# Optimization experiments

Measured on AMD Instinct MI355X. Metric: run time of the kernel, lower is better.

The kernel has to match this reference:

```python
import jax, jax.numpy as jnp
import numpy as np

T, D, F_, E, K = 8192, 1024, 4096, 8, 2


def setup_inputs() -> dict:
    key = jax.random.key(0)
    ks = jax.random.split(key, 5)
    s_d = 1.0 / np.sqrt(D)
    s_f = 1.0 / np.sqrt(F_)
    return {
        "x": jax.random.normal(ks[0], (T, D), dtype=jnp.float32),
        "gate_w": jax.random.normal(ks[1], (D, E), dtype=jnp.float32) * s_d,
        "w1": jax.random.normal(ks[2], (E, D, F_), dtype=jnp.float32) * s_d,  # up (gate proj)
        "w3": jax.random.normal(ks[3], (E, D, F_), dtype=jnp.float32) * s_d,  # up (value proj)
        "w2": jax.random.normal(ks[4], (E, F_, D), dtype=jnp.float32) * s_f,  # down proj
    }


def reference(x, gate_w, w1, w2, w3):
    # gate + top-k routing
    logits = x @ gate_w                                   # [T, E]
    top_w, top_idx = jax.lax.top_k(logits, K)             # [T, K]
    w = jax.nn.softmax(top_w.astype(jnp.float32), axis=-1).astype(x.dtype)
    # combine[t, e] = routing weight of token t for expert e (0 if unrouted)
    combine = jnp.sum(w[:, :, None] * jax.nn.one_hot(top_idx, E, dtype=x.dtype), axis=1)  # [T, E]
    # dense dispatch: each expert processes all tokens, masked by combine weight
    # (identical math to the torch gather/scatter loop: unrouted tokens get weight 0)
    out = jnp.zeros_like(x)
    for e in range(E):
        h = jax.nn.silu(x @ w1[e]) * (x @ w3[e])          # [T, F] SwiGLU
        out = out + combine[:, e:e + 1] * (h @ w2[e])     # [T, D]
    return out
```

## Files before the change

kernel.cpp:

```cpp
#include <hip/hip_runtime.h>
#include <stdint.h>

#define T_TOK 8192
#define D_DIM 1024
#define F_DIM 4096
#define E_NUM 8
#define RCAP  17408
#define MT    136

typedef __bf16 bf16;
typedef __bf16 bf16x8 __attribute__((ext_vector_type(8)));
typedef float  f32x4  __attribute__((ext_vector_type(4)));

typedef const __attribute__((address_space(1))) void* gptr1;
typedef __attribute__((address_space(3))) void* lptr3;

__device__ __forceinline__ void gload_lds16(const void* g, void* l) {
    __builtin_amdgcn_global_load_lds((gptr1)g, (lptr3)l, 16, 0, 0);
}

__device__ __forceinline__ unsigned short f2b(float f) {
    uint32_t u = __float_as_uint(f);
    u = (u + 0x7FFFu + ((u >> 16) & 1u)) >> 16;
    return (unsigned short)u;
}

__global__ __launch_bounds__(256) void trans_kernel(const float* __restrict__ src,
                                                    bf16* __restrict__ dst,
                                                    int R, int C, int mode) {
    __shared__ float lt[64 * 68];
    const int e  = blockIdx.z;
    const int c0 = blockIdx.x * 64;
    const int r0 = blockIdx.y * 64;
    const float* s = src + (size_t)e * R * C;
    unsigned short* dp = (unsigned short*)dst + (size_t)e * R * C * (mode ? 2 : 1);
    const int t  = threadIdx.x;
    const int tr = t >> 4;
    const int tc = (t & 15) * 4;
    #pragma unroll
    for (int rr = 0; rr < 4; ++rr) {
        const int r = tr + rr * 16;
        const float4 v = *(const float4*)(s + (size_t)(r0 + r) * C + c0 + tc);
        *(float4*)&lt[r * 68 + tc] = v;
    }
    __syncthreads();
    const int oc  = t >> 2;
    const int seg = (t & 3) * 16;
    __attribute__((aligned(16))) unsigned short ob[16];
    #pragma unroll
    for (int i = 0; i < 16; ++i) ob[i] = f2b(lt[(seg + i) * 68 + oc]);
    const int f  = c0 + oc;
    const int fr = mode ? ((f >> 5) * 64 + ((mode == 2) ? 32 : 0) + (f & 31)) : f;
    unsigned short* orow = dp + (size_t)fr * R + (r0 + seg);
    *(uint4*)(orow)     = *(const uint4*)&ob[0];
    *(uint4*)(orow + 8) = *(const uint4*)&ob[8];
}

__global__ __launch_bounds__(256) void gate_kernel(const float* __restrict__ x,
                                                   const float* __restrict__ gw,
                                                   int* __restrict__ tki,
                                                   float* __restrict__ tkw,
                                                   int* __restrict__ counts) {
    const int t    = blockIdx.x * 4 + (threadIdx.x >> 6);
    const int lane = threadIdx.x & 63;
    const float* xr = x + (size_t)t * D_DIM;
    float acc[E_NUM];
    #pragma unroll
    for (int e = 0; e < E_NUM; ++e) acc[e] = 0.f;
    for (int j = 0; j < 16; ++j) {
        const int d = lane + 64 * j;
        const float xv = xr[d];
        const float* g = gw + (size_t)d * E_NUM;
        #pragma unroll
        for (int e = 0; e < E_NUM; ++e) acc[e] += xv * g[e];
    }
    #pragma unroll
    for (int off = 32; off >= 1; off >>= 1) {
        #pragma unroll
        for (int e = 0; e < E_NUM; ++e) acc[e] += __shfl_xor(acc[e], off);
    }
    if (lane == 0) {
        int b0 = 0; float v0 = acc[0];
        #pragma unroll
        for (int e = 1; e < E_NUM; ++e) if (acc[e] > v0) { v0 = acc[e]; b0 = e; }
        int b1 = -1; float v1 = -1e30f;
        #pragma unroll
        for (int e = 0; e < E_NUM; ++e) if (e != b0 && acc[e] > v1) { v1 = acc[e]; b1 = e; }
        const float ex = expf(v1 - v0);
        const float w0 = 1.f / (1.f + ex);
        const float w1 = ex * w0;
        tki[t * 2]     = b0;  tkw[t * 2]     = w0;
        tki[t * 2 + 1] = b1;  tkw[t * 2 + 1] = w1;
        atomicAdd(&counts[b0], 1);
        atomicAdd(&counts[b1], 1);
    }
}

__global__ void scan_kernel(const int* __restrict__ counts, int* __restrict__ aoff,
                            int* __restrict__ cursor) {
    if (threadIdx.x == 0) {
        int off = 0;
        #pragma unroll
        for (int e = 0; e < E_NUM; ++e) {
            aoff[e]   = off;
            cursor[e] = off;
            off += (counts[e] + 127) & ~127;
        }
        aoff[E_NUM] = off;
    }
}

__global__ __launch_bounds__(256) void gather_kernel(const float* __restrict__ x,
                                                     const int* __restrict__ tki,
                                                     int* __restrict__ cursor,
                                                     int* __restrict__ s2r,
                                                     bf16* __restrict__ xp) {
    const int slot = blockIdx.x * 4 + (threadIdx.x >> 6);
    const int lane = threadIdx.x & 63;
    const int t = slot >> 1;
    int row = 0;
    if (lane == 0) {
        const int e = tki[slot];
        row = atomicAdd(&cursor[e], 1);
        s2r[slot] = row;
    }
    row = __shfl(row, 0);
    const float* xr = x + (size_t)t * D_DIM + lane * 16;
    unsigned short* dst = (unsigned short*)xp + (size_t)row * D_DIM + lane * 16;
    uint32_t u[8];
    #pragma unroll
    for (int q = 0; q < 4; ++q) {
        const float4 v = *(const float4*)(xr + q * 4);
        u[q * 2]     = (uint32_t)f2b(v.x) | ((uint32_t)f2b(v.y) << 16);
        u[q * 2 + 1] = (uint32_t)f2b(v.z) | ((uint32_t)f2b(v.w) << 16);
    }
    ((uint4*)dst)[0] = make_uint4(u[0], u[1], u[2], u[3]);
    ((uint4*)dst)[1] = make_uint4(u[4], u[5], u[6], u[7]);
}

__global__ __launch_bounds__(512, 2) void gemm1_kernel(const bf16* __restrict__ xp,
                                                       const bf16* __restrict__ wb13t,
                                                       bf16* __restrict__ hb,
                                                       const int* __restrict__ aoff,
                                                       const int* __restrict__ counts) {
    __shared__ __align__(16) char As[65536];
    __shared__ __align__(16) char Bs[65536];

    const int flat    = blockIdx.y * 32 + blockIdx.x;
    const int logical = (flat & 7) * 288 + (flat >> 3);
    const int nt      = logical & 31;
    int bm            = logical >> 5;

    int e = 0;
    for (; e < E_NUM; ++e) {
        const int nbi = (counts[e] + 255) >> 8;
        if (bm < nbi) break;
        bm -= nbi;
    }
    if (e >= E_NUM) return;
    const int m_base = aoff[e] + bm * 256;
    const int row_hi = aoff[e + 1];

    const int tid  = threadIdx.x;
    const int w    = tid >> 6;
    const int lane = tid & 63;
    const int wm   = w >> 2;
    const int wn   = w & 3;

    const int    lsub = lane >> 3;
    const size_t swz  = (size_t)(((lane & 7) ^ lsub) << 3);
    const bf16* Ag = xp    + (size_t)m_base * D_DIM;
    const bf16* Bg = wb13t + ((size_t)e * (2 * F_DIM) + (size_t)nt * 256) * D_DIM;
    char* sAd = As + w * 2048 + lane * 16;
    char* sBd = Bs + w * 2048 + lane * 16;
    const int rst = w * 16 + lsub;

#define G1_STAGE_A(cc, kt, h)                                                         \
    do {                                                                              \
        const size_t kcol = (size_t)(kt) * 64 + swz;                                  \
        gload_lds16(Ag + (size_t)((h) * 128 + rst) * D_DIM + kcol,                    \
                    sAd + (cc) * 32768 + (h) * 16384);                                \
        gload_lds16(Ag + (size_t)((h) * 128 + rst + 8) * D_DIM + kcol,                \
                    sAd + (cc) * 32768 + (h) * 16384 + 1024);                         \
    } while (0)
#define G1_STAGE_B(cc, kt, h)                                                         \
    do {                                                                              \
        const size_t kcol = (size_t)(kt) * 64 + swz;                                  \
        gload_lds16(Bg + (size_t)((h) * 128 + rst) * D_DIM + kcol,                    \
                    sBd + (cc) * 32768 + (h) * 16384);                                \
        gload_lds16(Bg + (size_t)((h) * 128 + rst + 8) * D_DIM + kcol,                \
                    sBd + (cc) * 32768 + (h) * 16384 + 1024);                         \
    } while (0)

    const int fm  = lane & 15;
    const int kq  = lane >> 4;
    const int kg0 = ((kq       ^ (fm & 7)) << 4);
    const int kg1 = (((4 | kq) ^ (fm & 7)) << 4);
    const char* Arb = As + wm * 16384 + fm * 128;
    const char* Brb = Bs + (wn >> 1) * 16384 + ((wn & 1) * 64 + fm) * 128;

    f32x4 acc[8][4] = {};
    bf16x8 aF[4][2], b0F[2][2], b1F[2][2];

    G1_STAGE_A(0, 0, 0); G1_STAGE_A(0, 0, 1);
    G1_STAGE_B(0, 0, 0); G1_STAGE_B(0, 0, 1);
    G1_STAGE_B(1, 1, 0); G1_STAGE_B(1, 1, 1);
    asm volatile("s_waitcnt vmcnt(4)" ::: "memory");
    __builtin_amdgcn_s_barrier();
    __builtin_amdgcn_sched_barrier(0);

    for (int u = 0; u < D_DIM / 64; ++u) {
        const int c = u & 1;
        const char* Ar = Arb + c * 32768;
        const char* Br = Brb + c * 32768;

        #pragma unroll
        for (int i = 0; i < 4; ++i) {
            aF[i][0] = *(const bf16x8*)(Ar + i * 2048 + kg0);
            aF[i][1] = *(const bf16x8*)(Ar + i * 2048 + kg1);
        }
        #pragma unroll
        for (int j = 0; j < 2; ++j) {
            b0F[j][0] = *(const bf16x8*)(Br + j * 2048 + kg0);
            b0F[j][1] = *(const bf16x8*)(Br + j * 2048 + kg1);
        }
        if (u + 1 < D_DIM / 64) G1_STAGE_A(c ^ 1, u + 1, 0);
        __builtin_amdgcn_s_barrier();
        asm volatile("s_waitcnt lgkmcnt(0)" ::: "memory");
        __builtin_amdgcn_s_setprio(1);
        #pragma unroll
        for (int i = 0; i < 4; ++i)
            #pragma unroll
            for (int j = 0; j < 2; ++j) {
                acc[i][j] = __builtin_amdgcn_mfma_f32_16x16x32_bf16(aF[i][0], b0F[j][0], acc[i][j], 0, 0, 0);
                acc[i][j] = __builtin_amdgcn_mfma_f32_16x16x32_bf16(aF[i][1], b0F[j][1], acc[i][j], 0, 0, 0);
            }
        __builtin_amdgcn_s_setprio(0);
        __builtin_amdgcn_s_barrier();

        #pragma unroll
        for (int j = 0; j < 2; ++j) {
            b1F[j][0] = *(const bf16x8*)(Br + (j + 2) * 2048 + kg0);
            b1F[j][1] = *(const bf16x8*)(Br + (j + 2) * 2048 + kg1);
        }
        if (u + 1 < D_DIM / 64) G1_STAGE_A(c ^ 1, u + 1, 1);
        __builtin_amdgcn_s_barrier();
        asm volatile("s_waitcnt lgkmcnt(0)" ::: "memory");
        __builtin_amdgcn_s_setprio(1);
        #pragma unroll
        for (int i = 0; i < 4; ++i)
            #pragma unroll
            for (int j = 0; j < 2; ++j) {
                acc[i][j + 2] = __builtin_amdgcn_mfma_f32_16x16x32_bf16(aF[i][0], b1F[j][0], acc[i][j + 2], 0, 0, 0);
                acc[i][j + 2] = __builtin_amdgcn_mfma_f32_16x16x32_bf16(aF[i][1], b1F[j][1], acc[i][j + 2], 0, 0, 0);
            }
        __builtin_amdgcn_s_setprio(0);
        __builtin_amdgcn_s_barrier();

        #pragma unroll
        for (int i = 0; i < 4; ++i) {
            aF[i][0] = *(const bf16x8*)(Ar + (i + 4) * 2048 + kg0);
            aF[i][1] = *(const bf16x8*)(Ar + (i + 4) * 2048 + kg1);
        }
        if (u + 2 < D_DIM / 64) G1_STAGE_B(c, u + 2, 0);
        __builtin_amdgcn_s_barrier();
        asm volatile("s_waitcnt lgkmcnt(0)" ::: "memory");
        __builtin_amdgcn_s_setprio(1);
        #pragma unroll
        for (int i = 0; i < 4; ++i)
            #pragma unroll
            for (int j = 0; j < 2; ++j) {
                acc[i + 4][j] = __builtin_amdgcn_mfma_f32_16x16x32_bf16(aF[i][0], b0F[j][0], acc[i + 4][j], 0, 0, 0);
                acc[i + 4][j] = __builtin_amdgcn_mfma_f32_16x16x32_bf16(aF[i][1], b0F[j][1], acc[i + 4][j], 0, 0, 0);
            }
        __builtin_amdgcn_s_setprio(0);
        __builtin_amdgcn_s_barrier();

        if (u + 2 < D_DIM / 64) G1_STAGE_B(c, u + 2, 1);
        __builtin_amdgcn_s_setprio(1);
        #pragma unroll
        for (int i = 0; i < 4; ++i)
            #pragma unroll
            for (int j = 0; j < 2; ++j) {
                acc[i + 4][j + 2] = __builtin_amdgcn_mfma_f32_16x16x32_bf16(aF[i][0], b1F[j][0], acc[i + 4][j + 2], 0, 0, 0);
                acc[i + 4][j + 2] = __builtin_amdgcn_mfma_f32_16x16x32_bf16(aF[i][1], b1F[j][1], acc[i + 4][j + 2], 0, 0, 0);
            }
        __builtin_amdgcn_s_setprio(0);

        if (u == D_DIM / 64 - 1) break;
        if (u + 2 < D_DIM / 64) {
            asm volatile("s_waitcnt vmcnt(4)" ::: "memory");
        } else {
            asm volatile("s_waitcnt vmcnt(0)" ::: "memory");
        }
        __builtin_amdgcn_s_barrier();
        __builtin_amdgcn_sched_barrier(0);
    }

    unsigned short* hw = (unsigned short*)hb;
    const int g    = nt * 4 + wn;
    const int colb = g * 32 + fm;
    const int rb0  = m_base + wm * 128 + (kq << 2);
    #pragma unroll
    for (int i = 0; i < 8; ++i) {
        #pragma unroll
        for (int r = 0; r < 4; ++r) {
            const int row = rb0 + i * 16 + r;
            if (row < row_hi) {
                #pragma unroll
                for (int jj = 0; jj < 2; ++jj) {
                    const float s1 = acc[i][jj][r];
                    const float s3 = acc[i][jj + 2][r];
                    const float hv = (s1 / (1.0f + __expf(-s1))) * s3;
                    hw[(size_t)row * F_DIM + colb + jj * 16] = f2b(hv);
                }
            }
        }
    }
#undef G1_STAGE_A
#undef G1_STAGE_B
}

__global__ __launch_bounds__(256, 2) void gemm2_kernel(const bf16* __restrict__ hb,
                                                       const bf16* __restrict__ wb2t,
                                                       float* __restrict__ yb,
                                                       const int* __restrict__ aoff,
                                                       const int* __restrict__ counts) {
    __shared__ bf16 As[128 * 32];
    __shared__ bf16 Bs[128 * 32];

    const int flat    = blockIdx.y * 8 + blockIdx.x;
    const int logical = (flat & 7) * 136 + (flat >> 3);
    const int nt      = logical & 7;
    const int m_base  = (logical >> 3) * 128;

    int e = 0;
    #pragma unroll
    for (int i = 1; i < E_NUM; ++i) if (m_base >= aoff[i]) e = i;
    if (m_base - aoff[e] >= counts[e]) return;

    const int tid  = threadIdx.x;
    const int w    = tid >> 6;
    const int lane = tid & 63;
    const int wm   = w & 1, wn = w >> 1;

    const bf16* Ab = hb + (size_t)m_base * F_DIM;
    const bf16* Bb = wb2t + ((size_t)e * D_DIM + (size_t)nt * 128) * F_DIM;

    const int lr16 = lane >> 2;
    const int cg   = lane & 3;
    const int srow = w * 32 + lr16;
    const int scol = (cg ^ ((lr16 >> 1) & 3)) * 8;
    const int ldsbase = w * 1024;
    const int fm = lane & 15;
    const int fk = (((lane >> 4) ^ ((fm >> 1) & 3))) * 8;

    f32x4 acc[4][4] = {};

    for (int kt = 0; kt < F_DIM / 32; ++kt) {
        const int k0 = kt * 32;
        #pragma unroll
        for (int j = 0; j < 2; ++j) {
            const size_t go = (size_t)(srow + j * 16) * F_DIM + (k0 + scol);
            gload_lds16(Ab + go, &As[ldsbase + j * 512]);
            gload_lds16(Bb + go, &Bs[ldsbase + j * 512]);
        }
        __syncthreads();
        bf16x8 af[4], bfr[4];
        #pragma unroll
        for (int i = 0; i < 4; ++i) {
            af[i]  = *(const bf16x8*)&As[(wm * 64 + i * 16 + fm) * 32 + fk];
            bfr[i] = *(const bf16x8*)&Bs[(wn * 64 + i * 16 + fm) * 32 + fk];
        }
        #pragma unroll
        for (int i = 0; i < 4; ++i) {
            #pragma unroll
            for (int jn = 0; jn < 4; ++jn) {
                acc[i][jn] = __builtin_amdgcn_mfma_f32_16x16x32_bf16(af[i], bfr[jn], acc[i][jn], 0, 0, 0);
            }
        }
        __syncthreads();
    }

    #pragma unroll
    for (int i = 0; i < 4; ++i) {
        const int rb = m_base + wm * 64 + i * 16 + (lane >> 4) * 4;
        #pragma unroll
        for (int r = 0; r < 4; ++r) {
            float* yrow = yb + (size_t)(rb + r) * D_DIM;
            #pragma unroll
            for (int jn = 0; jn < 4; ++jn) {
                const int col = nt * 128 + wn * 64 + jn * 16 + (lane & 15);
                yrow[col] = acc[i][jn][r];
            }
        }
    }
}

__global__ __launch_bounds__(256) void combine_kernel(const float* __restrict__ yb,
                                                      const int* __restrict__ s2r,
                                                      const float* __restrict__ tkw,
                                                      float* __restrict__ out) {
    const int idx = blockIdx.x * 256 + threadIdx.x;
    const int t = idx >> 8;
    const int c = (idx & 255) * 4;
    const int r0 = s2r[t * 2], r1 = s2r[t * 2 + 1];
    const float w0 = tkw[t * 2], w1 = tkw[t * 2 + 1];
    const float4 a = *(const float4*)(yb + (size_t)r0 * D_DIM + c);
    const float4 b = *(const float4*)(yb + (size_t)r1 * D_DIM + c);
    float4 o;
    o.x = w0 * a.x + w1 * b.x;
    o.y = w0 * a.y + w1 * b.y;
    o.z = w0 * a.z + w1 * b.z;
    o.w = w0 * a.w + w1 * b.w;
    *(float4*)(out + (size_t)t * D_DIM + c) = o;
}

extern "C" void kernel_launch(void* const* d_in, const int* in_sizes, int n_in,
                              void* d_out, int out_size, void* d_ws, size_t ws_size,
                              hipStream_t stream) {
    const float* x  = (const float*)d_in[0];
    const float* gw = (const float*)d_in[1];
    const float* w1 = (const float*)d_in[2];
    const float* w3 = (const float*)d_in[3];
    const float* w2 = (const float*)d_in[4];
    float* out = (float*)d_out;

    char* ws = (char*)d_ws;
    bf16*  wb13t = (bf16*)(ws);
    bf16*  wb2t  = (bf16*)(ws);
    float* yb    = (float*)(ws + (size_t)67108864);
    bf16*  xp    = (bf16*)(ws + (size_t)134217728);
    size_t off   = (size_t)134217728 + (size_t)RCAP * D_DIM * 2;
    bf16*  hb    = (bf16*)(ws + off); off += (size_t)RCAP * F_DIM * 2;
    int*   tki = (int*)(ws + off);   off += (size_t)T_TOK * 2 * 4;
    float* tkw = (float*)(ws + off); off += (size_t)T_TOK * 2 * 4;
    int* counts = (int*)(ws + off);  off += 64;
    int* cursor = (int*)(ws + off);  off += 64;
    int* aoff   = (int*)(ws + off);  off += 64;
    int* s2r    = (int*)(ws + off);  off += (size_t)T_TOK * 2 * 4;

    hipMemsetAsync(counts, 0, 64, stream);

    gate_kernel<<<T_TOK / 4, 256, 0, stream>>>(x, gw, tki, tkw, counts);
    scan_kernel<<<1, 64, 0, stream>>>(counts, aoff, cursor);
    gather_kernel<<<(T_TOK * 2) / 4, 256, 0, stream>>>(x, tki, cursor, s2r, xp);

    trans_kernel<<<dim3(F_DIM / 64, D_DIM / 64, E_NUM), 256, 0, stream>>>(w1, wb13t, D_DIM, F_DIM, 1);
    trans_kernel<<<dim3(F_DIM / 64, D_DIM / 64, E_NUM), 256, 0, stream>>>(w3, wb13t, D_DIM, F_DIM, 2);

    gemm1_kernel<<<dim3(2 * F_DIM / 256, 72), 512, 0, stream>>>(xp, wb13t, hb, aoff, counts);

    trans_kernel<<<dim3(D_DIM / 64, F_DIM / 64, E_NUM), 256, 0, stream>>>(w2, wb2t, F_DIM, D_DIM, 0);

    gemm2_kernel<<<dim3(D_DIM / 128, MT), 256, 0, stream>>>(hb, wb2t, yb, aoff, counts);

    combine_kernel<<<(T_TOK * 256) / 256, 256, 0, stream>>>(yb, s2r, tkw, out);
}
```

Baseline: 1.392 ms.

## Double gemm2 K-tile to 64 with XOR swizzle; drop gemm1 block remap

The gemm2 kernel now stages 64-wide K tiles per iteration instead of 32, which halves the number of barrier pairs. It switches to an 8-way XOR-swizzled LDS layout so that fragment reads avoid bank conflicts, and issues two MFMAs per accumulator per tile. The gemm1 kernel drops its grouped block-index remapping and uses blockIdx directly, which may lower L2 reuse of weight tiles across neighbouring blocks. The larger LDS footprint in gemm2 could reduce occupancy.

```diff
diff --git a/kernel.cpp b/kernel.cpp
--- a/kernel.cpp
+++ b/kernel.cpp
@@ -146,12 +146,9 @@
     __shared__ __align__(16) char As[65536];
     __shared__ __align__(16) char Bs[65536];
 
-    const int flat    = blockIdx.y * 32 + blockIdx.x;
-    const int logical = (flat & 7) * 288 + (flat >> 3);
-    const int nt      = logical & 31;
-    int bm            = logical >> 5;
-
-    int e = 0;
+    const int nt = blockIdx.x;
+    int bm = blockIdx.y;
+    int e  = 0;
     for (; e < E_NUM; ++e) {
         const int nbi = (counts[e] + 255) >> 8;
         if (bm < nbi) break;
@@ -326,8 +323,8 @@
                                                        float* __restrict__ yb,
                                                        const int* __restrict__ aoff,
                                                        const int* __restrict__ counts) {
-    __shared__ bf16 As[128 * 32];
-    __shared__ bf16 Bs[128 * 32];
+    __shared__ __align__(16) bf16 As[128 * 64];
+    __shared__ __align__(16) bf16 Bs[128 * 64];
 
     const int flat    = blockIdx.y * 8 + blockIdx.x;
     const int logical = (flat & 7) * 136 + (flat >> 3);
@@ -347,36 +344,43 @@
     const bf16* Ab = hb + (size_t)m_base * F_DIM;
     const bf16* Bb = wb2t + ((size_t)e * D_DIM + (size_t)nt * 128) * F_DIM;
 
-    const int lr16 = lane >> 2;
-    const int cg   = lane & 3;
-    const int srow = w * 32 + lr16;
-    const int scol = (cg ^ ((lr16 >> 1) & 3)) * 8;
-    const int ldsbase = w * 1024;
-    const int fm = lane & 15;
-    const int fk = (((lane >> 4) ^ ((fm >> 1) & 3))) * 8;
+    const int lsub = lane >> 3;
+    const int swzc = ((lane & 7) ^ lsub) * 8;
+    const int rst  = w * 32 + lsub;
+    bf16* sAd = As + w * 2048;
+    bf16* sBd = Bs + w * 2048;
+
+    const int fm  = lane & 15;
+    const int kq  = lane >> 4;
+    const int sl0 = ((kq    ) ^ (fm & 7)) * 8;
+    const int sl1 = ((kq | 4) ^ (fm & 7)) * 8;
 
     f32x4 acc[4][4] = {};
 
-    for (int kt = 0; kt < F_DIM / 32; ++kt) {
-        const int k0 = kt * 32;
-        #pragma unroll
-        for (int j = 0; j < 2; ++j) {
-            const size_t go = (size_t)(srow + j * 16) * F_DIM + (k0 + scol);
-            gload_lds16(Ab + go, &As[ldsbase + j * 512]);
-            gload_lds16(Bb + go, &Bs[ldsbase + j * 512]);
+    for (int kt = 0; kt < F_DIM / 64; ++kt) {
+        const int k0 = kt * 64;
+        #pragma unroll
+        for (int j = 0; j < 4; ++j) {
+            gload_lds16(Ab + (size_t)(rst + j * 8) * F_DIM + (k0 + swzc), sAd + j * 512);
+            gload_lds16(Bb + (size_t)(rst + j * 8) * F_DIM + (k0 + swzc), sBd + j * 512);
         }
         __syncthreads();
-        bf16x8 af[4], bfr[4];
+        bf16x8 af[4][2], bfr[4][2];
         #pragma unroll
         for (int i = 0; i < 4; ++i) {
-            af[i]  = *(const bf16x8*)&As[(wm * 64 + i * 16 + fm) * 32 + fk];
-            bfr[i] = *(const bf16x8*)&Bs[(wn * 64 + i * 16 + fm) * 32 + fk];
+            const int ar = (wm * 64 + i * 16 + fm) * 64;
+            const int br = (wn * 64 + i * 16 + fm) * 64;
+            af[i][0]  = *(const bf16x8*)&As[ar + sl0];
+            af[i][1]  = *(const bf16x8*)&As[ar + sl1];
+            bfr[i][0] = *(const bf16x8*)&Bs[br + sl0];
+            bfr[i][1] = *(const bf16x8*)&Bs[br + sl1];
         }
         #pragma unroll
         for (int i = 0; i < 4; ++i) {
             #pragma unroll
             for (int jn = 0; jn < 4; ++jn) {
-                acc[i][jn] = __builtin_amdgcn_mfma_f32_16x16x32_bf16(af[i], bfr[jn], acc[i][jn], 0, 0, 0);
+                acc[i][jn] = __builtin_amdgcn_mfma_f32_16x16x32_bf16(af[i][0], bfr[jn][0], acc[i][jn], 0, 0, 0);
+                acc[i][jn] = __builtin_amdgcn_mfma_f32_16x16x32_bf16(af[i][1], bfr[jn][1], acc[i][jn], 0, 0, 0);
             }
         }
         __syncthreads();
```

After: 1.345 ms. 1.03x faster.
